# Optimization experiments

Measured on AMD Instinct MI355X. Metric: run time of the kernel, lower is better.

The kernel has to match this reference:

```python
import jax, jax.numpy as jnp
import numpy as np

B, IN, H, L = 4096, 1024, 1024, 8


def setup_inputs() -> dict:
    key = jax.random.key(0)
    k1, k2, k3, k4, k5 = jax.random.split(key, 5)
    scale = 0.02
    inputs = jax.random.normal(k1, (B, IN), dtype=jnp.float32)
    # Stacked gate weights, order [f, i, o, g] along first axis (torch Linear: y = x @ W.T + b)
    W = jax.random.normal(k2, (4 * H, IN), dtype=jnp.float32) * scale   # input->gates
    bW = jax.random.normal(k3, (4 * H,), dtype=jnp.float32) * scale
    U = jax.random.normal(k4, (4 * H, H), dtype=jnp.float32) * scale    # hidden->gates
    bU = jax.random.normal(k5, (4 * H,), dtype=jnp.float32) * scale
    return {"inputs": inputs, "W": W, "bW": bW, "U": U, "bU": bU, "num_layers": L}


def reference(inputs, W, bW, U, bU, num_layers):
    batch = inputs.shape[0]
    hid = U.shape[1]
    # Input projection is loop-invariant: compute once. [B, 4H]
    x_proj = jnp.einsum('bi,gi->bg', inputs, W) + bW
    xf, xi, xo, xg = jnp.split(x_proj, 4, axis=1)

    def step(carry, _):
        ht, ct = carry
        h_proj = jnp.einsum('bh,gh->bg', ht, U) + bU  # [B, 4H]
        hf, hi, ho, hg = jnp.split(h_proj, 4, axis=1)
        f = jax.nn.sigmoid(xf + hf)
        i = jax.nn.sigmoid(xi + hi)
        o = jax.nn.sigmoid(xo + ho)
        g = jnp.tanh(xg + hg)
        ct_new = f * ct + i * g
        ht_new = o * jnp.tanh(ct_new)
        return (ht_new, ct_new), None

    h0 = jnp.zeros((batch, hid), dtype=inputs.dtype)
    c0 = jnp.zeros((batch, hid), dtype=inputs.dtype)
    (ht, ct), _ = jax.lax.scan(step, (h0, c0), None, length=num_layers)
    return ht, ct
```

## Files before the change

### kernel.cpp

```cpp
#include <hip/hip_runtime.h>
#include <hip/hip_bf16.h>

typedef __bf16 bf16x8 __attribute__((ext_vector_type(8)));
typedef float f32x4 __attribute__((ext_vector_type(4)));

#define DEVI static __device__ __forceinline__

DEVI void load_lds16(const void* g, void* l) {
  __builtin_amdgcn_global_load_lds(
      (const __attribute__((address_space(1))) void*)g,
      (__attribute__((address_space(3))) void*)l, 16, 0, 0);
}

DEVI unsigned short f2b(float f) { return __bfloat16_as_ushort(__float2bfloat16(f)); }
DEVI float b2f(unsigned short u) {
  union { unsigned int i; float f; } c;
  c.i = ((unsigned int)u) << 16;
  return c.f;
}
DEVI float sigm(float x) { return 1.0f / (1.0f + __expf(-x)); }
DEVI float tanh_fast(float x) { return 2.0f / (1.0f + __expf(-2.0f * x)) - 1.0f; }

DEVI int swz(int L) { return L ^ (((L >> 7) & 7) << 4); }

__global__ __launch_bounds__(256) void prep_kernel(
    const float* __restrict__ x, const float* __restrict__ W,
    const float* __restrict__ U, const float* __restrict__ bW,
    const float* __restrict__ bU, unsigned short* __restrict__ xb,
    unsigned short* __restrict__ Wbp, unsigned short* __restrict__ Ubp,
    float* __restrict__ bp) {
  const int bid = blockIdx.x;
  if (bid < 4096) {
    const int i = bid * 256 + threadIdx.x;
    const float4 v = reinterpret_cast<const float4*>(x)[i];
    ushort4 o;
    o.x = f2b(v.x); o.y = f2b(v.y); o.z = f2b(v.z); o.w = f2b(v.w);
    reinterpret_cast<ushort4*>(xb)[i] = o;
  } else if (bid < 12288) {
    const bool isW = bid < 8192;
    const float* src = isW ? W : U;
    unsigned short* dst = isW ? Wbp : Ubp;
    const int i = (bid - (isW ? 4096 : 8192)) * 256 + threadIdx.x;
    const int r = i >> 8;
    const int cw = i & 255;
    const float4 v = reinterpret_cast<const float4*>(src)[i];
    const int rp = ((r & 1023) << 2) + (r >> 10);
    ushort4 o;
    o.x = f2b(v.x); o.y = f2b(v.y); o.z = f2b(v.z); o.w = f2b(v.w);
    *reinterpret_cast<ushort4*>(&dst[(size_t)rp * 1024 + (cw << 2)]) = o;
  } else {
    const int i = (bid - 12288) * 256 + threadIdx.x;
    const int h = i >> 2, g = i & 3;
    bp[i] = bW[g * 1024 + h] + bU[g * 1024 + h];
  }
}

#define KPHASE(BFC, BFN, SLNXT, STAGEQ, DOSTAGE, WAITSTR, DOBAR)              \
  {                                                                           \
    if (DOSTAGE) STAGE(STAGEQ);                                               \
    const unsigned char* sln_ = (SLNXT);                                      \
    _Pragma("unroll") for (int n_ = 0; n_ < 4; ++n_)                          \
        BFN[n_] = *reinterpret_cast<const bf16x8*>(sln_ + offB[n_]);          \
    __builtin_amdgcn_s_setprio(1);                                            \
    _Pragma("unroll") for (int m_ = 0; m_ < 8; ++m_) {                        \
      _Pragma("unroll") for (int n_ = 0; n_ < 4; ++n_)                        \
          acc[m_][n_] = __builtin_amdgcn_mfma_f32_16x16x32_bf16(              \
              af[m_], BFC[n_], acc[m_][n_], 0, 0, 0);                         \
      af[m_] = *reinterpret_cast<const bf16x8*>(sln_ + offA[m_]);             \
    }                                                                         \
    __builtin_amdgcn_s_setprio(0);                                            \
    asm volatile(WAITSTR ::: "memory");                                       \
    __builtin_amdgcn_sched_barrier(0);                                        \
    if (DOBAR) {                                                              \
      __builtin_amdgcn_s_barrier();                                           \
      __builtin_amdgcn_sched_barrier(0);                                      \
    }                                                                         \
  }

template <int MODE>
__global__ __launch_bounds__(512, 2) void gemm256(
    const unsigned short* __restrict__ A,
    const unsigned short* __restrict__ Bm,
    const unsigned short* __restrict__ xpb_r,
    unsigned short* __restrict__ xpb_w,
    const float* __restrict__ bp,
    unsigned short* __restrict__ ct,
    unsigned short* __restrict__ htout,
    float* __restrict__ out) {
  constexpr int K = 1024, N = 4096;
  __shared__ unsigned char lds[256 * 528];

  const int tid = threadIdx.x;
  const int lane = tid & 63;
  const int wave = tid >> 6;
  const int wr = wave >> 2;
  const int wc = wave & 3;

  const int bid = blockIdx.x;
  const int sw = (bid & 7) * 32 + (bid >> 3);
  const int brow = (sw >> 4) * 256;
  const int bcol = (sw & 15) * 256;

  const int physA0 = tid * 16;
  const int physA1 = 8192 + tid * 16;
  const int physB0 = 16384 + tid * 16;
  const int physB1 = 24576 + tid * 16;
  const int LA0 = swz(physA0), LA1 = swz(physA1);
  const int LB0 = swz(physB0 - 16384), LB1 = swz(physB1 - 16384);
  const unsigned char* pA0 = (const unsigned char*)A + (size_t)(brow + (LA0 >> 6)) * (K * 2) + (LA0 & 63);
  const unsigned char* pA1 = (const unsigned char*)A + (size_t)(brow + (LA1 >> 6)) * (K * 2) + (LA1 & 63);
  const unsigned char* pB0 = (const unsigned char*)Bm + (size_t)(bcol + (LB0 >> 6)) * (K * 2) + (LB0 & 63);
  const unsigned char* pB1 = (const unsigned char*)Bm + (size_t)(bcol + (LB1 >> 6)) * (K * 2) + (LB1 & 63);

  const int s16 = (lane >> 4) * 16;
  int offA[8], offB[4];
#pragma unroll
  for (int m = 0; m < 8; ++m) {
    const int row = wr * 128 + m * 16 + (lane & 15);
    offA[m] = swz(row * 64 + s16);
  }
#pragma unroll
  for (int n = 0; n < 4; ++n) {
    const int row = wc * 64 + n * 16 + (lane & 15);
    offB[n] = 16384 + swz(row * 64 + s16);
  }

  f32x4 acc[8][4] = {};
  bf16x8 af[8], bfE[4], bfO[4];

  auto STAGE = [&](int q) {
    unsigned char* sb = lds + (q & 3) * 32768;
    const size_t kb = (size_t)q * 64;
    load_lds16(pA0 + kb, sb + physA0);
    load_lds16(pA1 + kb, sb + physA1);
    load_lds16(pB0 + kb, sb + physB0);
    load_lds16(pB1 + kb, sb + physB1);
  };

  STAGE(0); STAGE(1); STAGE(2); STAGE(3);
  asm volatile("s_waitcnt vmcnt(8)" ::: "memory");
  __builtin_amdgcn_s_barrier();
#pragma unroll
  for (int n = 0; n < 4; ++n) bfE[n] = *reinterpret_cast<const bf16x8*>(lds + offB[n]);
#pragma unroll
  for (int m = 0; m < 8; ++m) af[m] = *reinterpret_cast<const bf16x8*>(lds + offA[m]);
  asm volatile("s_waitcnt lgkmcnt(0)" ::: "memory");
  __builtin_amdgcn_sched_barrier(0);
  __builtin_amdgcn_s_barrier();
  __builtin_amdgcn_sched_barrier(0);

  for (int pp = 0; pp < 14; ++pp) {
    const int p = 2 * pp;
    const unsigned char* sl1 = lds + ((p + 1) & 3) * 32768;
    const unsigned char* sl2 = lds + ((p + 2) & 3) * 32768;
    KPHASE(bfE, bfO, sl1, p + 4, true, "s_waitcnt vmcnt(8) lgkmcnt(0)", true);
    KPHASE(bfO, bfE, sl2, p + 5, true, "s_waitcnt vmcnt(8) lgkmcnt(0)", true);
  }
  KPHASE(bfE, bfO, lds + (29 & 3) * 32768, 0, false, "s_waitcnt vmcnt(4) lgkmcnt(0)", true);
  KPHASE(bfO, bfE, lds + (30 & 3) * 32768, 0, false, "s_waitcnt vmcnt(0) lgkmcnt(0)", true);
  KPHASE(bfE, bfO, lds + (31 & 3) * 32768, 0, false, "s_waitcnt lgkmcnt(0)", false);
  __builtin_amdgcn_s_setprio(1);
#pragma unroll
  for (int m = 0; m < 8; ++m)
#pragma unroll
    for (int n = 0; n < 4; ++n)
      acc[m][n] = __builtin_amdgcn_mfma_f32_16x16x32_bf16(af[m], bfO[n], acc[m][n], 0, 0, 0);
  __builtin_amdgcn_s_setprio(0);

  __syncthreads();
  unsigned short* cs = (unsigned short*)lds;
  {
    const int c0 = wc * 64 + (lane & 15);
    const int r00 = wr * 128 + ((lane >> 4) << 2);
#pragma unroll
    for (int m = 0; m < 8; ++m)
#pragma unroll
      for (int n = 0; n < 4; ++n) {
        const int rr = r00 + m * 16;
        const int cc = c0 + n * 16;
#pragma unroll
        for (int r = 0; r < 4; ++r) cs[(rr + r) * 264 + cc] = f2b(acc[m][n][r]);
      }
  }
  __syncthreads();

  const int hbase = bcol >> 2;
#pragma unroll 2
  for (int j = 0; j < 8; ++j) {
    const int v = tid + (j << 9);
    const int row = v >> 4;
    const int h4 = (v & 15) << 2;
    const int ci = (brow + row) * 1024 + hbase + h4;

    unsigned short pvv[16];
    *reinterpret_cast<uint4*>(&pvv[0]) = *reinterpret_cast<const uint4*>(&cs[row * 264 + h4 * 4]);
    *reinterpret_cast<uint4*>(&pvv[8]) = *reinterpret_cast<const uint4*>(&cs[row * 264 + h4 * 4 + 8]);

    float sf[4], si_[4], so_[4], sg_[4];
    if constexpr (MODE == 0) {
      float bpf[16];
#pragma unroll
      for (int q = 0; q < 4; ++q)
        *reinterpret_cast<float4*>(&bpf[q * 4]) =
            *reinterpret_cast<const float4*>(&bp[bcol + h4 * 4 + q * 4]);
#pragma unroll
      for (int k = 0; k < 4; ++k) {
        sf[k] = b2f(pvv[4 * k + 0]) + bpf[4 * k + 0];
        si_[k] = b2f(pvv[4 * k + 1]) + bpf[4 * k + 1];
        so_[k] = b2f(pvv[4 * k + 2]) + bpf[4 * k + 2];
        sg_[k] = b2f(pvv[4 * k + 3]) + bpf[4 * k + 3];
      }
      unsigned short xo[16];
#pragma unroll
      for (int k = 0; k < 4; ++k) {
        xo[4 * k + 0] = f2b(sf[k]);
        xo[4 * k + 1] = f2b(si_[k]);
        xo[4 * k + 2] = f2b(so_[k]);
        xo[4 * k + 3] = f2b(sg_[k]);
      }
      unsigned short* xw = &xpb_w[(size_t)(brow + row) * N + bcol + h4 * 4];
      *reinterpret_cast<uint4*>(xw) = *reinterpret_cast<const uint4*>(&xo[0]);
      *reinterpret_cast<uint4*>(xw + 8) = *reinterpret_cast<const uint4*>(&xo[8]);
    } else {
      unsigned short xvv[16];
      const unsigned short* xr = &xpb_r[(size_t)(brow + row) * N + bcol + h4 * 4];
      *reinterpret_cast<uint4*>(&xvv[0]) = *reinterpret_cast<const uint4*>(xr);
      *reinterpret_cast<uint4*>(&xvv[8]) = *reinterpret_cast<const uint4*>(xr + 8);
#pragma unroll
      for (int k = 0; k < 4; ++k) {
        sf[k] = b2f(pvv[4 * k + 0]) + b2f(xvv[4 * k + 0]);
        si_[k] = b2f(pvv[4 * k + 1]) + b2f(xvv[4 * k + 1]);
        so_[k] = b2f(pvv[4 * k + 2]) + b2f(xvv[4 * k + 2]);
        sg_[k] = b2f(pvv[4 * k + 3]) + b2f(xvv[4 * k + 3]);
      }
    }

    float c_old[4] = {0.f, 0.f, 0.f, 0.f};
    if constexpr (MODE != 0) {
      const ushort4 cv = *reinterpret_cast<const ushort4*>(&ct[ci]);
      c_old[0] = b2f(cv.x); c_old[1] = b2f(cv.y);
      c_old[2] = b2f(cv.z); c_old[3] = b2f(cv.w);
    }

    float cn[4], hn[4];
#pragma unroll
    for (int k = 0; k < 4; ++k) {
      const float f = sigm(sf[k]);
      const float ii = sigm(si_[k]);
      const float o = sigm(so_[k]);
      const float gg = tanh_fast(sg_[k]);
      const float c = fmaf(f, c_old[k], ii * gg);
      cn[k] = c;
      hn[k] = o * tanh_fast(c);
    }

    if constexpr (MODE == 2) {
      *reinterpret_cast<float4*>(&out[ci]) = make_float4(hn[0], hn[1], hn[2], hn[3]);
      *reinterpret_cast<float4*>(&out[4194304 + ci]) = make_float4(cn[0], cn[1], cn[2], cn[3]);
    } else {
      ushort4 cb, hb;
      cb.x = f2b(cn[0]); cb.y = f2b(cn[1]); cb.z = f2b(cn[2]); cb.w = f2b(cn[3]);
      hb.x = f2b(hn[0]); hb.y = f2b(hn[1]); hb.z = f2b(hn[2]); hb.w = f2b(hn[3]);
      *reinterpret_cast<ushort4*>(&ct[ci]) = cb;
      *reinterpret_cast<ushort4*>(&htout[ci]) = hb;
    }
  }
}

extern "C" void kernel_launch(void* const* d_in, const int* in_sizes, int n_in,
                              void* d_out, int out_size, void* d_ws, size_t ws_size,
                              hipStream_t stream) {
  const float* x = (const float*)d_in[0];
  const float* W = (const float*)d_in[1];
  const float* bW = (const float*)d_in[2];
  const float* U = (const float*)d_in[3];
  const float* bU = (const float*)d_in[4];
  float* out = (float*)d_out;

  char* w = (char*)d_ws;
  const size_t MB = 1ull << 20;
  unsigned short* xb = (unsigned short*)(w + 0 * MB);
  unsigned short* Wbp = (unsigned short*)(w + 8 * MB);
  unsigned short* Ubp = (unsigned short*)(w + 16 * MB);
  unsigned short* xpb = (unsigned short*)(w + 24 * MB);
  unsigned short* ct = (unsigned short*)(w + 56 * MB);
  unsigned short* htA = (unsigned short*)(w + 64 * MB);
  unsigned short* htB = (unsigned short*)(w + 72 * MB);
  float* bp = (float*)(w + 80 * MB);

  prep_kernel<<<12304, 256, 0, stream>>>(x, W, U, bW, bU, xb, Wbp, Ubp, bp);

  gemm256<0><<<256, 512, 0, stream>>>(xb, Wbp, nullptr, xpb, bp, ct, htA, nullptr);

  const unsigned short* hin = htA;
  unsigned short* hout = htB;
  for (int t = 1; t <= 6; ++t) {
    gemm256<1><<<256, 512, 0, stream>>>(hin, Ubp, xpb, nullptr, nullptr, ct, hout, nullptr);
    const unsigned short* tmp = hout;
    hout = (unsigned short*)hin;
    hin = tmp;
  }
  gemm256<2><<<256, 512, 0, stream>>>(hin, Ubp, xpb, nullptr, nullptr, ct, nullptr, out);
}
```

Measured before the change: 370.4 us.

## Run recurrent GEMMs in FP8 with scaled operands and pre-permuted K layout

Converts U and the hidden state to FP8 (E4M3) with fixed power-of-two scales and runs the seven recurrent GEMMs with fp8 MFMA over half as many K phases. The hidden state is written straight into an FP8 image with a K-permutation that matches the MFMA operand layout, and the first step is specialised into its own kernel. The goal is to halve operand bytes and double matrix throughput for the recurrence. The cost is lower precision, a software float-to-fp8 conversion in the epilogue, and possible accuracy-tolerance risk.

```diff
diff --git a/kernel.cpp b/kernel.cpp
--- a/kernel.cpp
+++ b/kernel.cpp
@@ -3,6 +3,7 @@
 
 typedef __bf16 bf16x8 __attribute__((ext_vector_type(8)));
 typedef float f32x4 __attribute__((ext_vector_type(4)));
+typedef long i64x2 __attribute__((ext_vector_type(2)));
 
 #define DEVI static __device__ __forceinline__
 
@@ -21,13 +22,36 @@
 DEVI float sigm(float x) { return 1.0f / (1.0f + __expf(-x)); }
 DEVI float tanh_fast(float x) { return 2.0f / (1.0f + __expf(-2.0f * x)) - 1.0f; }
 
+DEVI unsigned char f2fp8(float f) {
+  const unsigned int u = __float_as_uint(f);
+  const unsigned char s = (unsigned char)((u >> 24) & 0x80);
+  const float a = fabsf(f);
+  if (a >= 448.f) return s | 0x7E;
+  if (a < 0.015625f) {
+    const int M = (int)rintf(a * 512.f);
+    if (M > 7) return s | 0x08;
+    return s | (unsigned char)M;
+  }
+  int ex;
+  const float m = frexpf(a, &ex);
+  int r = (int)rintf(m * 16.f);
+  if (r == 16) { r = 8; ex += 1; }
+  const int E = ex + 6, M = r - 8;
+  if (E > 15 || (E == 15 && M == 7)) return s | 0x7E;
+  return s | (unsigned char)((E << 3) | M);
+}
+
 DEVI int swz(int L) { return L ^ (((L >> 7) & 7) << 4); }
+
+DEVI int imgk(int hc) {
+  return (hc & ~63) + (((hc >> 3) & 3) << 4) + (((hc >> 5) & 1) << 3) + (hc & 7);
+}
 
 __global__ __launch_bounds__(256) void prep_kernel(
     const float* __restrict__ x, const float* __restrict__ W,
     const float* __restrict__ U, const float* __restrict__ bW,
     const float* __restrict__ bU, unsigned short* __restrict__ xb,
-    unsigned short* __restrict__ Wbp, unsigned short* __restrict__ Ubp,
+    unsigned short* __restrict__ Wbp, unsigned char* __restrict__ Up8,
     float* __restrict__ bp) {
   const int bid = blockIdx.x;
   if (bid < 4096) {
@@ -36,20 +60,39 @@
     ushort4 o;
     o.x = f2b(v.x); o.y = f2b(v.y); o.z = f2b(v.z); o.w = f2b(v.w);
     reinterpret_cast<ushort4*>(xb)[i] = o;
-  } else if (bid < 12288) {
-    const bool isW = bid < 8192;
-    const float* src = isW ? W : U;
-    unsigned short* dst = isW ? Wbp : Ubp;
-    const int i = (bid - (isW ? 4096 : 8192)) * 256 + threadIdx.x;
+  } else if (bid < 8192) {
+    const int i = (bid - 4096) * 256 + threadIdx.x;
     const int r = i >> 8;
     const int cw = i & 255;
-    const float4 v = reinterpret_cast<const float4*>(src)[i];
+    const float4 v = reinterpret_cast<const float4*>(W)[i];
     const int rp = ((r & 1023) << 2) + (r >> 10);
     ushort4 o;
     o.x = f2b(v.x); o.y = f2b(v.y); o.z = f2b(v.z); o.w = f2b(v.w);
-    *reinterpret_cast<ushort4*>(&dst[(size_t)rp * 1024 + (cw << 2)]) = o;
+    *reinterpret_cast<ushort4*>(&Wbp[(size_t)rp * 1024 + (cw << 2)]) = o;
+  } else if (bid < 9216) {
+    const int i = (bid - 8192) * 256 + threadIdx.x;
+    const int d0 = i << 4;
+    const int rp = d0 >> 10;
+    const int ik0 = d0 & 1023;
+    const int P = ik0 >> 6, q = (ik0 >> 4) & 3;
+    const int k0 = P * 64 + q * 8;
+    const int srcrow = (rp & 3) * 1024 + (rp >> 2);
+    const float* S = U + (size_t)srcrow * 1024;
+    const float4 a0 = *reinterpret_cast<const float4*>(S + k0);
+    const float4 a1 = *reinterpret_cast<const float4*>(S + k0 + 4);
+    const float4 b0 = *reinterpret_cast<const float4*>(S + k0 + 32);
+    const float4 b1 = *reinterpret_cast<const float4*>(S + k0 + 36);
+    auto pk = [](unsigned char a, unsigned char b, unsigned char c, unsigned char d) {
+      return (unsigned)a | ((unsigned)b << 8) | ((unsigned)c << 16) | ((unsigned)d << 24);
+    };
+    uint4 w;
+    w.x = pk(f2fp8(a0.x * 32.f), f2fp8(a0.y * 32.f), f2fp8(a0.z * 32.f), f2fp8(a0.w * 32.f));
+    w.y = pk(f2fp8(a1.x * 32.f), f2fp8(a1.y * 32.f), f2fp8(a1.z * 32.f), f2fp8(a1.w * 32.f));
+    w.z = pk(f2fp8(b0.x * 32.f), f2fp8(b0.y * 32.f), f2fp8(b0.z * 32.f), f2fp8(b0.w * 32.f));
+    w.w = pk(f2fp8(b1.x * 32.f), f2fp8(b1.y * 32.f), f2fp8(b1.z * 32.f), f2fp8(b1.w * 32.f));
+    *reinterpret_cast<uint4*>(&Up8[d0]) = w;
   } else {
-    const int i = (bid - 12288) * 256 + threadIdx.x;
+    const int i = (bid - 9216) * 256 + threadIdx.x;
     const int h = i >> 2, g = i & 3;
     bp[i] = bW[g * 1024 + h] + bU[g * 1024 + h];
   }
@@ -77,53 +120,43 @@
     }                                                                         \
   }
 
-template <int MODE>
-__global__ __launch_bounds__(512, 2) void gemm256(
+__global__ __launch_bounds__(512, 2) void gemm_x(
     const unsigned short* __restrict__ A,
     const unsigned short* __restrict__ Bm,
-    const unsigned short* __restrict__ xpb_r,
     unsigned short* __restrict__ xpb_w,
     const float* __restrict__ bp,
     unsigned short* __restrict__ ct,
-    unsigned short* __restrict__ htout,
-    float* __restrict__ out) {
+    unsigned char* __restrict__ htimg) {
   constexpr int K = 1024, N = 4096;
+  constexpr int NPH = K / 32;
   __shared__ unsigned char lds[256 * 528];
 
   const int tid = threadIdx.x;
   const int lane = tid & 63;
   const int wave = tid >> 6;
-  const int wr = wave >> 2;
-  const int wc = wave & 3;
-
+  const int wr = wave >> 2, wc = wave & 3;
   const int bid = blockIdx.x;
   const int sw = (bid & 7) * 32 + (bid >> 3);
-  const int brow = (sw >> 4) * 256;
-  const int bcol = (sw & 15) * 256;
-
-  const int physA0 = tid * 16;
-  const int physA1 = 8192 + tid * 16;
-  const int physB0 = 16384 + tid * 16;
-  const int physB1 = 24576 + tid * 16;
-  const int LA0 = swz(physA0), LA1 = swz(physA1);
-  const int LB0 = swz(physB0 - 16384), LB1 = swz(physB1 - 16384);
+  const int brow = (sw >> 4) * 256, bcol = (sw & 15) * 256;
+
+  const int physA0 = tid * 16, physA1 = 8192 + tid * 16;
+  const int physB0 = 16384 + tid * 16, physB1 = 24576 + tid * 16;
+  const int LA0 = swz(physA0), LA1 = swz(physA1 - 8192) + 0;
+  const int LA1r = swz(8192 + tid * 16);
+  const int LB0 = swz(tid * 16), LB1 = swz(8192 + tid * 16);
   const unsigned char* pA0 = (const unsigned char*)A + (size_t)(brow + (LA0 >> 6)) * (K * 2) + (LA0 & 63);
-  const unsigned char* pA1 = (const unsigned char*)A + (size_t)(brow + (LA1 >> 6)) * (K * 2) + (LA1 & 63);
+  const unsigned char* pA1 = (const unsigned char*)A + (size_t)(brow + (LA1r >> 6)) * (K * 2) + (LA1r & 63);
   const unsigned char* pB0 = (const unsigned char*)Bm + (size_t)(bcol + (LB0 >> 6)) * (K * 2) + (LB0 & 63);
   const unsigned char* pB1 = (const unsigned char*)Bm + (size_t)(bcol + (LB1 >> 6)) * (K * 2) + (LB1 & 63);
 
   const int s16 = (lane >> 4) * 16;
   int offA[8], offB[4];
 #pragma unroll
-  for (int m = 0; m < 8; ++m) {
-    const int row = wr * 128 + m * 16 + (lane & 15);
-    offA[m] = swz(row * 64 + s16);
-  }
-#pragma unroll
-  for (int n = 0; n < 4; ++n) {
-    const int row = wc * 64 + n * 16 + (lane & 15);
-    offB[n] = 16384 + swz(row * 64 + s16);
-  }
+  for (int m = 0; m < 8; ++m)
+    offA[m] = swz((wr * 128 + m * 16 + (lane & 15)) * 64 + s16);
+#pragma unroll
+  for (int n = 0; n < 4; ++n)
+    offB[n] = 16384 + swz((wc * 64 + n * 16 + (lane & 15)) * 64 + s16);
 
   f32x4 acc[8][4] = {};
   bf16x8 af[8], bfE[4], bfO[4];
@@ -176,8 +209,7 @@
     for (int m = 0; m < 8; ++m)
 #pragma unroll
       for (int n = 0; n < 4; ++n) {
-        const int rr = r00 + m * 16;
-        const int cc = c0 + n * 16;
+        const int rr = r00 + m * 16, cc = c0 + n * 16;
 #pragma unroll
         for (int r = 0; r < 4; ++r) cs[(rr + r) * 264 + cc] = f2b(acc[m][n][r]);
       }
@@ -196,73 +228,217 @@
     *reinterpret_cast<uint4*>(&pvv[0]) = *reinterpret_cast<const uint4*>(&cs[row * 264 + h4 * 4]);
     *reinterpret_cast<uint4*>(&pvv[8]) = *reinterpret_cast<const uint4*>(&cs[row * 264 + h4 * 4 + 8]);
 
+    float bpf[16];
+#pragma unroll
+    for (int q = 0; q < 4; ++q)
+      *reinterpret_cast<float4*>(&bpf[q * 4]) =
+          *reinterpret_cast<const float4*>(&bp[bcol + h4 * 4 + q * 4]);
+
     float sf[4], si_[4], so_[4], sg_[4];
-    if constexpr (MODE == 0) {
-      float bpf[16];
-#pragma unroll
-      for (int q = 0; q < 4; ++q)
-        *reinterpret_cast<float4*>(&bpf[q * 4]) =
-            *reinterpret_cast<const float4*>(&bp[bcol + h4 * 4 + q * 4]);
-#pragma unroll
-      for (int k = 0; k < 4; ++k) {
-        sf[k] = b2f(pvv[4 * k + 0]) + bpf[4 * k + 0];
-        si_[k] = b2f(pvv[4 * k + 1]) + bpf[4 * k + 1];
-        so_[k] = b2f(pvv[4 * k + 2]) + bpf[4 * k + 2];
-        sg_[k] = b2f(pvv[4 * k + 3]) + bpf[4 * k + 3];
-      }
-      unsigned short xo[16];
-#pragma unroll
-      for (int k = 0; k < 4; ++k) {
-        xo[4 * k + 0] = f2b(sf[k]);
-        xo[4 * k + 1] = f2b(si_[k]);
-        xo[4 * k + 2] = f2b(so_[k]);
-        xo[4 * k + 3] = f2b(sg_[k]);
-      }
-      unsigned short* xw = &xpb_w[(size_t)(brow + row) * N + bcol + h4 * 4];
-      *reinterpret_cast<uint4*>(xw) = *reinterpret_cast<const uint4*>(&xo[0]);
-      *reinterpret_cast<uint4*>(xw + 8) = *reinterpret_cast<const uint4*>(&xo[8]);
-    } else {
-      unsigned short xvv[16];
-      const unsigned short* xr = &xpb_r[(size_t)(brow + row) * N + bcol + h4 * 4];
-      *reinterpret_cast<uint4*>(&xvv[0]) = *reinterpret_cast<const uint4*>(xr);
-      *reinterpret_cast<uint4*>(&xvv[8]) = *reinterpret_cast<const uint4*>(xr + 8);
-#pragma unroll
-      for (int k = 0; k < 4; ++k) {
-        sf[k] = b2f(pvv[4 * k + 0]) + b2f(xvv[4 * k + 0]);
-        si_[k] = b2f(pvv[4 * k + 1]) + b2f(xvv[4 * k + 1]);
-        so_[k] = b2f(pvv[4 * k + 2]) + b2f(xvv[4 * k + 2]);
-        sg_[k] = b2f(pvv[4 * k + 3]) + b2f(xvv[4 * k + 3]);
-      }
+    unsigned short xo[16];
+#pragma unroll
+    for (int k = 0; k < 4; ++k) {
+      sf[k] = b2f(pvv[4 * k + 0]) + bpf[4 * k + 0];
+      si_[k] = b2f(pvv[4 * k + 1]) + bpf[4 * k + 1];
+      so_[k] = b2f(pvv[4 * k + 2]) + bpf[4 * k + 2];
+      sg_[k] = b2f(pvv[4 * k + 3]) + bpf[4 * k + 3];
+      xo[4 * k + 0] = f2b(sf[k]);
+      xo[4 * k + 1] = f2b(si_[k]);
+      xo[4 * k + 2] = f2b(so_[k]);
+      xo[4 * k + 3] = f2b(sg_[k]);
     }
-
-    float c_old[4] = {0.f, 0.f, 0.f, 0.f};
-    if constexpr (MODE != 0) {
-      const ushort4 cv = *reinterpret_cast<const ushort4*>(&ct[ci]);
-      c_old[0] = b2f(cv.x); c_old[1] = b2f(cv.y);
-      c_old[2] = b2f(cv.z); c_old[3] = b2f(cv.w);
-    }
+    unsigned short* xw = &xpb_w[(size_t)(brow + row) * N + bcol + h4 * 4];
+    *reinterpret_cast<uint4*>(xw) = *reinterpret_cast<const uint4*>(&xo[0]);
+    *reinterpret_cast<uint4*>(xw + 8) = *reinterpret_cast<const uint4*>(&xo[8]);
 
     float cn[4], hn[4];
 #pragma unroll
     for (int k = 0; k < 4; ++k) {
-      const float f = sigm(sf[k]);
       const float ii = sigm(si_[k]);
       const float o = sigm(so_[k]);
       const float gg = tanh_fast(sg_[k]);
+      const float c = ii * gg;
+      cn[k] = c;
+      hn[k] = o * tanh_fast(c);
+    }
+    ushort4 cb;
+    cb.x = f2b(cn[0]); cb.y = f2b(cn[1]); cb.z = f2b(cn[2]); cb.w = f2b(cn[3]);
+    *reinterpret_cast<ushort4*>(&ct[ci]) = cb;
+    const int hc0 = hbase + h4;
+    uchar4 h8;
+    h8.x = f2fp8(hn[0] * 16.f); h8.y = f2fp8(hn[1] * 16.f);
+    h8.z = f2fp8(hn[2] * 16.f); h8.w = f2fp8(hn[3] * 16.f);
+    *reinterpret_cast<uchar4*>(&htimg[(size_t)(brow + row) * 1024 + imgk(hc0)]) = h8;
+  }
+}
+
+#define KPHASE8(BFC, BFN, SLNXT, STAGEQ, DOSTAGE, WAITSTR, DOBAR)             \
+  {                                                                           \
+    if (DOSTAGE) STAGE(STAGEQ);                                               \
+    const unsigned char* sln_ = (SLNXT);                                      \
+    _Pragma("unroll") for (int n_ = 0; n_ < 4; ++n_)                          \
+        BFN[n_] = *reinterpret_cast<const i64x2*>(sln_ + offB[n_]);           \
+    __builtin_amdgcn_s_setprio(1);                                            \
+    _Pragma("unroll") for (int m_ = 0; m_ < 8; ++m_) {                        \
+      _Pragma("unroll") for (int n_ = 0; n_ < 4; ++n_)                        \
+          acc[m_][n_] = __builtin_amdgcn_mfma_f32_16x16x32_fp8_fp8(           \
+              af[m_][0], BFC[n_][0], acc[m_][n_], 0, 0, 0);                   \
+      _Pragma("unroll") for (int n_ = 0; n_ < 4; ++n_)                        \
+          acc[m_][n_] = __builtin_amdgcn_mfma_f32_16x16x32_fp8_fp8(           \
+              af[m_][1], BFC[n_][1], acc[m_][n_], 0, 0, 0);                   \
+      af[m_] = *reinterpret_cast<const i64x2*>(sln_ + offA[m_]);              \
+    }                                                                         \
+    __builtin_amdgcn_s_setprio(0);                                            \
+    asm volatile(WAITSTR ::: "memory");                                       \
+    __builtin_amdgcn_sched_barrier(0);                                        \
+    if (DOBAR) {                                                              \
+      __builtin_amdgcn_s_barrier();                                           \
+      __builtin_amdgcn_sched_barrier(0);                                      \
+    }                                                                         \
+  }
+
+template <bool LAST>
+__global__ __launch_bounds__(512, 2) void gemm_r(
+    const unsigned char* __restrict__ Aimg,
+    const unsigned char* __restrict__ Bimg,
+    const unsigned short* __restrict__ xpb_r,
+    unsigned short* __restrict__ ct,
+    unsigned char* __restrict__ htimg,
+    float* __restrict__ out) {
+  constexpr int N = 4096;
+  constexpr int NPH = 16;
+  __shared__ unsigned char lds[256 * 528];
+
+  const int tid = threadIdx.x;
+  const int lane = tid & 63;
+  const int wave = tid >> 6;
+  const int wr = wave >> 2, wc = wave & 3;
+  const int bid = blockIdx.x;
+  const int sw = (bid & 7) * 32 + (bid >> 3);
+  const int brow = (sw >> 4) * 256, bcol = (sw & 15) * 256;
+
+  const int physA0 = tid * 16, physA1 = 8192 + tid * 16;
+  const int physB0 = 16384 + tid * 16, physB1 = 24576 + tid * 16;
+  const int LA0 = swz(tid * 16), LA1 = swz(8192 + tid * 16);
+  const unsigned char* pA0 = Aimg + (size_t)(brow + (LA0 >> 6)) * 1024 + (LA0 & 63);
+  const unsigned char* pA1 = Aimg + (size_t)(brow + (LA1 >> 6)) * 1024 + (LA1 & 63);
+  const unsigned char* pB0 = Bimg + (size_t)(bcol + (LA0 >> 6)) * 1024 + (LA0 & 63);
+  const unsigned char* pB1 = Bimg + (size_t)(bcol + (LA1 >> 6)) * 1024 + (LA1 & 63);
+
+  const int s16 = (lane >> 4) * 16;
+  int offA[8], offB[4];
+#pragma unroll
+  for (int m = 0; m < 8; ++m)
+    offA[m] = swz((wr * 128 + m * 16 + (lane & 15)) * 64 + s16);
+#pragma unroll
+  for (int n = 0; n < 4; ++n)
+    offB[n] = 16384 + swz((wc * 64 + n * 16 + (lane & 15)) * 64 + s16);
+
+  f32x4 acc[8][4] = {};
+  i64x2 af[8], bfE[4], bfO[4];
+
+  auto STAGE = [&](int q) {
+    unsigned char* sb = lds + (q & 3) * 32768;
+    const size_t kb = (size_t)q * 64;
+    load_lds16(pA0 + kb, sb + physA0);
+    load_lds16(pA1 + kb, sb + physA1);
+    load_lds16(pB0 + kb, sb + physB0);
+    load_lds16(pB1 + kb, sb + physB1);
+  };
+
+  STAGE(0); STAGE(1); STAGE(2); STAGE(3);
+  asm volatile("s_waitcnt vmcnt(8)" ::: "memory");
+  __builtin_amdgcn_s_barrier();
+#pragma unroll
+  for (int n = 0; n < 4; ++n) bfE[n] = *reinterpret_cast<const i64x2*>(lds + offB[n]);
+#pragma unroll
+  for (int m = 0; m < 8; ++m) af[m] = *reinterpret_cast<const i64x2*>(lds + offA[m]);
+  asm volatile("s_waitcnt lgkmcnt(0)" ::: "memory");
+  __builtin_amdgcn_sched_barrier(0);
+  __builtin_amdgcn_s_barrier();
+  __builtin_amdgcn_sched_barrier(0);
+
+  for (int pp = 0; pp < 6; ++pp) {
+    const int p = 2 * pp;
+    const unsigned char* sl1 = lds + ((p + 1) & 3) * 32768;
+    const unsigned char* sl2 = lds + ((p + 2) & 3) * 32768;
+    KPHASE8(bfE, bfO, sl1, p + 4, true, "s_waitcnt vmcnt(8) lgkmcnt(0)", true);
+    KPHASE8(bfO, bfE, sl2, p + 5, true, "s_waitcnt vmcnt(8) lgkmcnt(0)", true);
+  }
+  KPHASE8(bfE, bfO, lds + (13 & 3) * 32768, 0, false, "s_waitcnt vmcnt(4) lgkmcnt(0)", true);
+  KPHASE8(bfO, bfE, lds + (14 & 3) * 32768, 0, false, "s_waitcnt vmcnt(0) lgkmcnt(0)", true);
+  KPHASE8(bfE, bfO, lds + (15 & 3) * 32768, 0, false, "s_waitcnt lgkmcnt(0)", false);
+  __builtin_amdgcn_s_setprio(1);
+#pragma unroll
+  for (int m = 0; m < 8; ++m) {
+#pragma unroll
+    for (int n = 0; n < 4; ++n)
+      acc[m][n] = __builtin_amdgcn_mfma_f32_16x16x32_fp8_fp8(af[m][0], bfO[n][0], acc[m][n], 0, 0, 0);
+#pragma unroll
+    for (int n = 0; n < 4; ++n)
+      acc[m][n] = __builtin_amdgcn_mfma_f32_16x16x32_fp8_fp8(af[m][1], bfO[n][1], acc[m][n], 0, 0, 0);
+  }
+  __builtin_amdgcn_s_setprio(0);
+
+  __syncthreads();
+  unsigned short* cs = (unsigned short*)lds;
+  {
+    const float inv = 1.0f / 512.0f;
+    const int c0 = wc * 64 + (lane & 15);
+    const int r00 = wr * 128 + ((lane >> 4) << 2);
+#pragma unroll
+    for (int m = 0; m < 8; ++m)
+#pragma unroll
+      for (int n = 0; n < 4; ++n) {
+        const int rr = r00 + m * 16, cc = c0 + n * 16;
+#pragma unroll
+        for (int r = 0; r < 4; ++r) cs[(rr + r) * 264 + cc] = f2b(acc[m][n][r] * inv);
+      }
+  }
+  __syncthreads();
+
+  const int hbase = bcol >> 2;
+#pragma unroll 2
+  for (int j = 0; j < 8; ++j) {
+    const int v = tid + (j << 9);
+    const int row = v >> 4;
+    const int h4 = (v & 15) << 2;
+    const int ci = (brow + row) * 1024 + hbase + h4;
+
+    unsigned short pvv[16], xvv[16];
+    *reinterpret_cast<uint4*>(&pvv[0]) = *reinterpret_cast<const uint4*>(&cs[row * 264 + h4 * 4]);
+    *reinterpret_cast<uint4*>(&pvv[8]) = *reinterpret_cast<const uint4*>(&cs[row * 264 + h4 * 4 + 8]);
+    const unsigned short* xr = &xpb_r[(size_t)(brow + row) * N + bcol + h4 * 4];
+    *reinterpret_cast<uint4*>(&xvv[0]) = *reinterpret_cast<const uint4*>(xr);
+    *reinterpret_cast<uint4*>(&xvv[8]) = *reinterpret_cast<const uint4*>(xr + 8);
+
+    const ushort4 cv = *reinterpret_cast<const ushort4*>(&ct[ci]);
+    float c_old[4] = {b2f(cv.x), b2f(cv.y), b2f(cv.z), b2f(cv.w)};
+
+    float cn[4], hn[4];
+#pragma unroll
+    for (int k = 0; k < 4; ++k) {
+      const float f = sigm(b2f(pvv[4 * k + 0]) + b2f(xvv[4 * k + 0]));
+      const float ii = sigm(b2f(pvv[4 * k + 1]) + b2f(xvv[4 * k + 1]));
+      const float o = sigm(b2f(pvv[4 * k + 2]) + b2f(xvv[4 * k + 2]));
+      const float gg = tanh_fast(b2f(pvv[4 * k + 3]) + b2f(xvv[4 * k + 3]));
       const float c = fmaf(f, c_old[k], ii * gg);
       cn[k] = c;
       hn[k] = o * tanh_fast(c);
     }
 
-    if constexpr (MODE == 2) {
+    if constexpr (LAST) {
       *reinterpret_cast<float4*>(&out[ci]) = make_float4(hn[0], hn[1], hn[2], hn[3]);
       *reinterpret_cast<float4*>(&out[4194304 + ci]) = make_float4(cn[0], cn[1], cn[2], cn[3]);
     } else {
-      ushort4 cb, hb;
+      ushort4 cb;
       cb.x = f2b(cn[0]); cb.y = f2b(cn[1]); cb.z = f2b(cn[2]); cb.w = f2b(cn[3]);
-      hb.x = f2b(hn[0]); hb.y = f2b(hn[1]); hb.z = f2b(hn[2]); hb.w = f2b(hn[3]);
       *reinterpret_cast<ushort4*>(&ct[ci]) = cb;
-      *reinterpret_cast<ushort4*>(&htout[ci]) = hb;
+      const int hc0 = hbase + h4;
+      uchar4 h8;
+      h8.x = f2fp8(hn[0] * 16.f); h8.y = f2fp8(hn[1] * 16.f);
+      h8.z = f2fp8(hn[2] * 16.f); h8.w = f2fp8(hn[3] * 16.f);
+      *reinterpret_cast<uchar4*>(&htimg[(size_t)(brow + row) * 1024 + imgk(hc0)]) = h8;
     }
   }
 }
@@ -281,24 +457,24 @@
   const size_t MB = 1ull << 20;
   unsigned short* xb = (unsigned short*)(w + 0 * MB);
   unsigned short* Wbp = (unsigned short*)(w + 8 * MB);
-  unsigned short* Ubp = (unsigned short*)(w + 16 * MB);
+  unsigned char* Up8 = (unsigned char*)(w + 16 * MB);
   unsigned short* xpb = (unsigned short*)(w + 24 * MB);
   unsigned short* ct = (unsigned short*)(w + 56 * MB);
-  unsigned short* htA = (unsigned short*)(w + 64 * MB);
-  unsigned short* htB = (unsigned short*)(w + 72 * MB);
-  float* bp = (float*)(w + 80 * MB);
-
-  prep_kernel<<<12304, 256, 0, stream>>>(x, W, U, bW, bU, xb, Wbp, Ubp, bp);
-
-  gemm256<0><<<256, 512, 0, stream>>>(xb, Wbp, nullptr, xpb, bp, ct, htA, nullptr);
-
-  const unsigned short* hin = htA;
-  unsigned short* hout = htB;
+  unsigned char* htA = (unsigned char*)(w + 64 * MB);
+  unsigned char* htB = (unsigned char*)(w + 68 * MB);
+  float* bp = (float*)(w + 72 * MB);
+
+  prep_kernel<<<9232, 256, 0, stream>>>(x, W, U, bW, bU, xb, Wbp, Up8, bp);
+
+  gemm_x<<<256, 512, 0, stream>>>(xb, Wbp, xpb, bp, ct, htA);
+
+  const unsigned char* hin = htA;
+  unsigned char* hout = htB;
   for (int t = 1; t <= 6; ++t) {
-    gemm256<1><<<256, 512, 0, stream>>>(hin, Ubp, xpb, nullptr, nullptr, ct, hout, nullptr);
-    const unsigned short* tmp = hout;
-    hout = (unsigned short*)hin;
+    gemm_r<false><<<256, 512, 0, stream>>>(hin, Up8, xpb, ct, hout, nullptr);
+    const unsigned char* tmp = hout;
+    hout = (unsigned char*)hin;
     hin = tmp;
   }
-  gemm256<2><<<256, 512, 0, stream>>>(hin, Ubp, xpb, nullptr, nullptr, ct, nullptr, out);
-}
+  gemm_r<true><<<256, 512, 0, stream>>>(hin, Up8, xpb, ct, nullptr, out);
+}
```

New measurement: 360.3 us. 2.7% less time.
